# Optimization experiments

Hardware: AMD Instinct MI355X
Metric: run time of the kernel (lower is better)

The kernel has to match this reference:

```python
import jax, jax.numpy as jnp
import numpy as np

N_NODES = 100000
N_EDGES = 2000000
D = 128
REL_TYPES = 64


def setup_inputs() -> dict:
    key = jax.random.key(0)
    k1, k2, k3, k4 = jax.random.split(key, 4)
    z = jax.random.normal(k1, (N_NODES, D), dtype=jnp.float32)
    edge_index = jax.random.randint(k2, (2, N_EDGES), 0, N_NODES, dtype=jnp.int64)
    rel_id = jax.random.randint(k3, (N_EDGES,), 0, REL_TYPES, dtype=jnp.int64)
    rel = jax.random.normal(k4, (REL_TYPES, D), dtype=jnp.float32)
    return {"z": z, "edge_index": edge_index, "rel_id": rel_id, "rel": rel}


def reference(z, edge_index, rel_id, rel):
    # DistMult: sigmoid(sum_d z[src,d] * rel[rel_id,d] * z[dst,d])
    src = z[edge_index[0]]          # [E, D]
    dst = z[edge_index[1]]          # [E, D]
    r = rel[rel_id]                 # [E, D]
    scores = jnp.sum(src * r * dst, axis=1)  # [E]
    return jax.nn.sigmoid(scores)
```

## Files before the change

kernel.cpp:

```cpp
#include <hip/hip_runtime.h>
#include <hip/hip_fp16.h>
#include <stdint.h>


__global__ __launch_bounds__(256) void convert_kernel(
    const float* __restrict__ x, __half* __restrict__ xh, int n8)
{
    const int i = blockIdx.x * blockDim.x + threadIdx.x;
    if (i >= n8) return;
    const float4 f0 = ((const float4*)x)[2 * i];
    const float4 f1 = ((const float4*)x)[2 * i + 1];
    union { __half2 h2[4]; uint4 u; } o;
    o.h2[0] = __floats2half2_rn(f0.x, f0.y);
    o.h2[1] = __floats2half2_rn(f0.z, f0.w);
    o.h2[2] = __floats2half2_rn(f1.x, f1.y);
    o.h2[3] = __floats2half2_rn(f1.z, f1.w);
    ((uint4*)xh)[i] = o.u;
}

__global__ __launch_bounds__(256) void distmult_f16_lds_kernel(
    const __half* __restrict__ zh,
    const int* __restrict__ src_idx,
    const int* __restrict__ dst_idx,
    const int* __restrict__ rel_id,
    const __half* __restrict__ relh,
    float* __restrict__ out,
    int E)
{
    __shared__ uint4 rel_lds[1024];
    {
        const uint4* rsrc = (const uint4*)relh;
        #pragma unroll
        for (int k = 0; k < 4; k++)
            rel_lds[threadIdx.x + 256 * k] = rsrc[threadIdx.x + 256 * k];
    }
    __syncthreads();

    const int gtid = blockIdx.x * blockDim.x + threadIdx.x;
    const int g    = gtid >> 4;
    const int lane = threadIdx.x & 15;
    const int e0   = g * 2;
    const int e1   = e0 + 1;
    if (e0 >= E) return;
    const bool has1 = (e1 < E);

    const int s0 = src_idx[e0], d0 = dst_idx[e0], r0 = rel_id[e0];
    const int s1 = has1 ? src_idx[e1] : s0;
    const int d1 = has1 ? dst_idx[e1] : d0;
    const int r1 = has1 ? rel_id[e1]  : r0;

    union { uint4 u; __half2 h2[4]; } A0, B0, A1, B1, R0, R1;
    A0.u = ((const uint4*)(zh + (size_t)s0 * 128))[lane];
    B0.u = ((const uint4*)(zh + (size_t)d0 * 128))[lane];
    A1.u = ((const uint4*)(zh + (size_t)s1 * 128))[lane];
    B1.u = ((const uint4*)(zh + (size_t)d1 * 128))[lane];
    R0.u = rel_lds[r0 * 16 + lane];
    R1.u = rel_lds[r1 * 16 + lane];

    float v0 = 0.f, v1 = 0.f;
    #pragma unroll
    for (int j = 0; j < 4; j++) {
        const float2 a0 = __half22float2(A0.h2[j]);
        const float2 b0 = __half22float2(B0.h2[j]);
        const float2 r0f = __half22float2(R0.h2[j]);
        v0 += a0.x * r0f.x * b0.x + a0.y * r0f.y * b0.y;
        const float2 a1 = __half22float2(A1.h2[j]);
        const float2 b1 = __half22float2(B1.h2[j]);
        const float2 r1f = __half22float2(R1.h2[j]);
        v1 += a1.x * r1f.x * b1.x + a1.y * r1f.y * b1.y;
    }

    #pragma unroll
    for (int off = 8; off > 0; off >>= 1) {
        v0 += __shfl_down(v0, off, 16);
        v1 += __shfl_down(v1, off, 16);
    }

    if (lane == 0) {
        const float o0 = 1.0f / (1.0f + __expf(-v0));
        if (has1) {
            const float o1 = 1.0f / (1.0f + __expf(-v1));
            *((float2*)(out + e0)) = make_float2(o0, o1);
        } else {
            out[e0] = o0;
        }
    }
}

__global__ __launch_bounds__(256) void distmult_f16_kernel(
    const __half* __restrict__ zh,
    const int* __restrict__ src_idx, const int* __restrict__ dst_idx,
    const int* __restrict__ rel_id, const float* __restrict__ rel,
    float* __restrict__ out, int E)
{
    const int gtid = blockIdx.x * blockDim.x + threadIdx.x;
    const int e = gtid >> 4;
    const int lane = threadIdx.x & 15;
    if (e >= E) return;
    const int s = src_idx[e], d = dst_idx[e], r = rel_id[e];
    union { uint4 u; __half2 h2[4]; } A, B;
    A.u = ((const uint4*)(zh + (size_t)s * 128))[lane];
    B.u = ((const uint4*)(zh + (size_t)d * 128))[lane];
    const float4* rr = (const float4*)(rel + (size_t)r * 128);
    const float4 r0 = rr[2 * lane];
    const float4 r1 = rr[2 * lane + 1];
    const float2 a0 = __half22float2(A.h2[0]), a1 = __half22float2(A.h2[1]);
    const float2 a2 = __half22float2(A.h2[2]), a3 = __half22float2(A.h2[3]);
    const float2 b0 = __half22float2(B.h2[0]), b1 = __half22float2(B.h2[1]);
    const float2 b2 = __half22float2(B.h2[2]), b3 = __half22float2(B.h2[3]);
    float v = a0.x * r0.x * b0.x + a0.y * r0.y * b0.y
            + a1.x * r0.z * b1.x + a1.y * r0.w * b1.y
            + a2.x * r1.x * b2.x + a2.y * r1.y * b2.y
            + a3.x * r1.z * b3.x + a3.y * r1.w * b3.y;
    #pragma unroll
    for (int off = 8; off > 0; off >>= 1) v += __shfl_down(v, off, 16);
    if (lane == 0) out[e] = 1.0f / (1.0f + __expf(-v));
}

__global__ __launch_bounds__(256) void distmult_f32_kernel(
    const float* __restrict__ z,
    const int* __restrict__ src_idx, const int* __restrict__ dst_idx,
    const int* __restrict__ rel_id, const float* __restrict__ rel,
    float* __restrict__ out, int E)
{
    const int gtid = blockIdx.x * blockDim.x + threadIdx.x;
    const int e = gtid >> 4;
    const int lane = threadIdx.x & 15;
    if (e >= E) return;
    const int s = src_idx[e], d = dst_idx[e], r = rel_id[e];
    const float4* zs = (const float4*)(z + (size_t)s * 128);
    const float4* zd = (const float4*)(z + (size_t)d * 128);
    const float4* rr = (const float4*)(rel + (size_t)r * 128);
    const float4 a0 = zs[lane], a1 = zs[lane + 16];
    const float4 b0 = zd[lane], b1 = zd[lane + 16];
    const float4 c0 = rr[lane], c1 = rr[lane + 16];
    float v = a0.x * c0.x * b0.x + a0.y * c0.y * b0.y
            + a0.z * c0.z * b0.z + a0.w * c0.w * b0.w
            + a1.x * c1.x * b1.x + a1.y * c1.y * b1.y
            + a1.z * c1.z * b1.z + a1.w * c1.w * b1.w;
    #pragma unroll
    for (int off = 8; off > 0; off >>= 1) v += __shfl_down(v, off, 16);
    if (lane == 0) out[e] = 1.0f / (1.0f + __expf(-v));
}

extern "C" void kernel_launch(void* const* d_in, const int* in_sizes, int n_in,
                              void* d_out, int out_size, void* d_ws, size_t ws_size,
                              hipStream_t stream) {
    const float* z     = (const float*)d_in[0];
    const int*   eidx  = (const int*)d_in[1];
    const int*   relid = (const int*)d_in[2];
    const float* rel   = (const float*)d_in[3];
    float*       out   = (float*)d_out;

    const int nz   = in_sizes[0];
    const int E    = in_sizes[2];
    const int nrel = in_sizes[3];
    const int* src = eidx;
    const int* dst = eidx + E;

    const size_t sz_zh   = (size_t)nz * sizeof(__half);
    const size_t off_rh  = (sz_zh + 255) & ~(size_t)255;
    const size_t sz_rh   = (size_t)nrel * sizeof(__half);
    const size_t need    = off_rh + sz_rh;

    const bool rel_ok = (nrel == 64 * 128) && (nrel % 8 == 0);

    if (ws_size >= need && nz % 8 == 0 && rel_ok) {
        __half* zh = (__half*)d_ws;
        __half* rh = (__half*)((char*)d_ws + off_rh);
        const int n8z = nz / 8, n8r = nrel / 8;
        convert_kernel<<<(n8z + 255) / 256, 256, 0, stream>>>(z, zh, n8z);
        convert_kernel<<<(n8r + 255) / 256, 256, 0, stream>>>(rel, rh, n8r);
        const int groups = (E + 1) / 2;
        const int blocks = (groups * 16 + 255) / 256;
        distmult_f16_lds_kernel<<<blocks, 256, 0, stream>>>(
            zh, src, dst, relid, rh, out, E);
    } else if (ws_size >= sz_zh && nz % 8 == 0) {
        __half* zh = (__half*)d_ws;
        const int n8z = nz / 8;
        convert_kernel<<<(n8z + 255) / 256, 256, 0, stream>>>(z, zh, n8z);
        const int blocks = (E * 16 + 255) / 256;
        distmult_f16_kernel<<<blocks, 256, 0, stream>>>(zh, src, dst, relid, rel, out, E);
    } else {
        const int blocks = (E * 16 + 255) / 256;
        distmult_f32_kernel<<<blocks, 256, 0, stream>>>(z, src, dst, relid, rel, out, E);
    }
}
```

Measured before the change: 225.6 us.

## Bucket edges by src/dst node range to improve gather cache locality

Adds a scatter pass that bins edges into 512 buckets keyed by source-range and destination-range, packing src, dst, rel and edge id into 64-bit words. The compute kernel then walks each bucket so concurrently running blocks touch a limited slice of the fp16 node table, aiming to raise L2/MALL hit rates for the random row gathers. In exchange it adds an atomic-heavy scatter pass, extra 16 MB of binned traffic, scattered output writes, and silently drops edges if a bucket exceeds its fixed capacity.

```diff
diff --git a/kernel.cpp b/kernel.cpp
--- a/kernel.cpp
+++ b/kernel.cpp
@@ -2,6 +2,10 @@
 #include <hip/hip_fp16.h>
 #include <stdint.h>
 
+
+#define NSRC 8
+#define NDST 64
+#define NBKT 512
 
 __global__ __launch_bounds__(256) void convert_kernel(
     const float* __restrict__ x, __half* __restrict__ xh, int n8)
@@ -18,36 +22,71 @@
     ((uint4*)xh)[i] = o.u;
 }
 
-__global__ __launch_bounds__(256) void distmult_f16_lds_kernel(
+__global__ __launch_bounds__(256) void scatter512_kernel(
+    const int* __restrict__ src, const int* __restrict__ dst,
+    const int* __restrict__ relid, int E, int nn, int cap,
+    uint32_t* __restrict__ counters, uint64_t* __restrict__ binned)
+{
+    const int i = blockIdx.x * 256 + threadIdx.x;
+    if (i >= E) return;
+    const uint32_t s = (uint32_t)src[i];
+    const uint32_t d = (uint32_t)dst[i];
+    const uint32_t r = (uint32_t)relid[i];
+    uint32_t ss = (s * (uint32_t)NSRC) / (uint32_t)nn; if (ss > NSRC - 1) ss = NSRC - 1;
+    uint32_t ds = (d * (uint32_t)NDST) / (uint32_t)nn; if (ds > NDST - 1) ds = NDST - 1;
+    const uint32_t b = ss * NDST + ds;
+    const uint32_t pos = atomicAdd(&counters[b], 1u);
+    if (pos < (uint32_t)cap)
+        binned[(size_t)b * (size_t)cap + pos] =
+            (uint64_t)s | ((uint64_t)d << 17) | ((uint64_t)r << 34) | ((uint64_t)i << 40);
+}
+
+__global__ __launch_bounds__(256) void distmult_bucketed_kernel(
     const __half* __restrict__ zh,
-    const int* __restrict__ src_idx,
-    const int* __restrict__ dst_idx,
-    const int* __restrict__ rel_id,
+    const uint64_t* __restrict__ binned,
+    const uint32_t* __restrict__ counters,
     const __half* __restrict__ relh,
     float* __restrict__ out,
-    int E)
-{
+    int cap, int cpb)
+{
+    const int k     = blockIdx.x & 7;
+    const int t     = blockIdx.x >> 3;
+    const int j     = t / cpb;
+    const int chunk = t - j * cpb;
+    const int bkt   = k * NDST + j;
+
+    uint32_t cnt = counters[bkt];
+    if (cnt > (uint32_t)cap) cnt = (uint32_t)cap;
+    const uint32_t el_blk = (uint32_t)chunk * 32u;
+    if (el_blk >= cnt) return;
+
     __shared__ uint4 rel_lds[1024];
     {
         const uint4* rsrc = (const uint4*)relh;
         #pragma unroll
-        for (int k = 0; k < 4; k++)
-            rel_lds[threadIdx.x + 256 * k] = rsrc[threadIdx.x + 256 * k];
+        for (int q = 0; q < 4; q++)
+            rel_lds[threadIdx.x + 256 * q] = rsrc[threadIdx.x + 256 * q];
     }
     __syncthreads();
 
-    const int gtid = blockIdx.x * blockDim.x + threadIdx.x;
-    const int g    = gtid >> 4;
+    const int g    = threadIdx.x >> 4;
     const int lane = threadIdx.x & 15;
-    const int e0   = g * 2;
-    const int e1   = e0 + 1;
-    if (e0 >= E) return;
-    const bool has1 = (e1 < E);
-
-    const int s0 = src_idx[e0], d0 = dst_idx[e0], r0 = rel_id[e0];
-    const int s1 = has1 ? src_idx[e1] : s0;
-    const int d1 = has1 ? dst_idx[e1] : d0;
-    const int r1 = has1 ? rel_id[e1]  : r0;
+    const uint32_t el0 = el_blk + (uint32_t)g * 2u;
+    if (el0 >= cnt) return;
+    const bool has1 = (el0 + 1u < cnt);
+
+    const uint64_t* bb = binned + (size_t)bkt * (size_t)cap;
+    const uint64_t p0 = bb[el0];
+    const uint64_t p1 = has1 ? bb[el0 + 1u] : p0;
+
+    const uint32_t s0 = (uint32_t)p0 & 0x1FFFFu;
+    const uint32_t d0 = (uint32_t)(p0 >> 17) & 0x1FFFFu;
+    const uint32_t r0 = (uint32_t)(p0 >> 34) & 0x3Fu;
+    const uint32_t e0 = (uint32_t)(p0 >> 40);
+    const uint32_t s1 = (uint32_t)p1 & 0x1FFFFu;
+    const uint32_t d1 = (uint32_t)(p1 >> 17) & 0x1FFFFu;
+    const uint32_t r1 = (uint32_t)(p1 >> 34) & 0x3Fu;
+    const uint32_t e1 = (uint32_t)(p1 >> 40);
 
     union { uint4 u; __half2 h2[4]; } A0, B0, A1, B1, R0, R1;
     A0.u = ((const uint4*)(zh + (size_t)s0 * 128))[lane];
@@ -59,15 +98,15 @@
 
     float v0 = 0.f, v1 = 0.f;
     #pragma unroll
-    for (int j = 0; j < 4; j++) {
-        const float2 a0 = __half22float2(A0.h2[j]);
-        const float2 b0 = __half22float2(B0.h2[j]);
-        const float2 r0f = __half22float2(R0.h2[j]);
-        v0 += a0.x * r0f.x * b0.x + a0.y * r0f.y * b0.y;
-        const float2 a1 = __half22float2(A1.h2[j]);
-        const float2 b1 = __half22float2(B1.h2[j]);
-        const float2 r1f = __half22float2(R1.h2[j]);
-        v1 += a1.x * r1f.x * b1.x + a1.y * r1f.y * b1.y;
+    for (int q = 0; q < 4; q++) {
+        const float2 a0 = __half22float2(A0.h2[q]);
+        const float2 b0 = __half22float2(B0.h2[q]);
+        const float2 c0 = __half22float2(R0.h2[q]);
+        v0 += a0.x * c0.x * b0.x + a0.y * c0.y * b0.y;
+        const float2 a1 = __half22float2(A1.h2[q]);
+        const float2 b1 = __half22float2(B1.h2[q]);
+        const float2 c1 = __half22float2(R1.h2[q]);
+        v1 += a1.x * c1.x * b1.x + a1.y * c1.y * b1.y;
     }
 
     #pragma unroll
@@ -76,6 +115,64 @@
         v1 += __shfl_down(v1, off, 16);
     }
 
+    if (lane == 0) {
+        out[e0] = 1.0f / (1.0f + __expf(-v0));
+        if (has1) out[e1] = 1.0f / (1.0f + __expf(-v1));
+    }
+}
+
+__global__ __launch_bounds__(256) void distmult_f16_lds_kernel(
+    const __half* __restrict__ zh,
+    const int* __restrict__ src_idx, const int* __restrict__ dst_idx,
+    const int* __restrict__ rel_id, const __half* __restrict__ relh,
+    float* __restrict__ out, int E)
+{
+    __shared__ uint4 rel_lds[1024];
+    {
+        const uint4* rsrc = (const uint4*)relh;
+        #pragma unroll
+        for (int q = 0; q < 4; q++)
+            rel_lds[threadIdx.x + 256 * q] = rsrc[threadIdx.x + 256 * q];
+    }
+    __syncthreads();
+
+    const int gtid = blockIdx.x * blockDim.x + threadIdx.x;
+    const int g = gtid >> 4;
+    const int lane = threadIdx.x & 15;
+    const int e0 = g * 2, e1 = e0 + 1;
+    if (e0 >= E) return;
+    const bool has1 = (e1 < E);
+
+    const int s0 = src_idx[e0], d0 = dst_idx[e0], r0 = rel_id[e0];
+    const int s1 = has1 ? src_idx[e1] : s0;
+    const int d1 = has1 ? dst_idx[e1] : d0;
+    const int r1 = has1 ? rel_id[e1]  : r0;
+
+    union { uint4 u; __half2 h2[4]; } A0, B0, A1, B1, R0, R1;
+    A0.u = ((const uint4*)(zh + (size_t)s0 * 128))[lane];
+    B0.u = ((const uint4*)(zh + (size_t)d0 * 128))[lane];
+    A1.u = ((const uint4*)(zh + (size_t)s1 * 128))[lane];
+    B1.u = ((const uint4*)(zh + (size_t)d1 * 128))[lane];
+    R0.u = rel_lds[r0 * 16 + lane];
+    R1.u = rel_lds[r1 * 16 + lane];
+
+    float v0 = 0.f, v1 = 0.f;
+    #pragma unroll
+    for (int q = 0; q < 4; q++) {
+        const float2 a0 = __half22float2(A0.h2[q]);
+        const float2 b0 = __half22float2(B0.h2[q]);
+        const float2 c0 = __half22float2(R0.h2[q]);
+        v0 += a0.x * c0.x * b0.x + a0.y * c0.y * b0.y;
+        const float2 a1 = __half22float2(A1.h2[q]);
+        const float2 b1 = __half22float2(B1.h2[q]);
+        const float2 c1 = __half22float2(R1.h2[q]);
+        v1 += a1.x * c1.x * b1.x + a1.y * c1.y * b1.y;
+    }
+    #pragma unroll
+    for (int off = 8; off > 0; off >>= 1) {
+        v0 += __shfl_down(v0, off, 16);
+        v1 += __shfl_down(v1, off, 16);
+    }
     if (lane == 0) {
         const float o0 = 1.0f / (1.0f + __expf(-v0));
         if (has1) {
@@ -85,36 +182,6 @@
             out[e0] = o0;
         }
     }
-}
-
-__global__ __launch_bounds__(256) void distmult_f16_kernel(
-    const __half* __restrict__ zh,
-    const int* __restrict__ src_idx, const int* __restrict__ dst_idx,
-    const int* __restrict__ rel_id, const float* __restrict__ rel,
-    float* __restrict__ out, int E)
-{
-    const int gtid = blockIdx.x * blockDim.x + threadIdx.x;
-    const int e = gtid >> 4;
-    const int lane = threadIdx.x & 15;
-    if (e >= E) return;
-    const int s = src_idx[e], d = dst_idx[e], r = rel_id[e];
-    union { uint4 u; __half2 h2[4]; } A, B;
-    A.u = ((const uint4*)(zh + (size_t)s * 128))[lane];
-    B.u = ((const uint4*)(zh + (size_t)d * 128))[lane];
-    const float4* rr = (const float4*)(rel + (size_t)r * 128);
-    const float4 r0 = rr[2 * lane];
-    const float4 r1 = rr[2 * lane + 1];
-    const float2 a0 = __half22float2(A.h2[0]), a1 = __half22float2(A.h2[1]);
-    const float2 a2 = __half22float2(A.h2[2]), a3 = __half22float2(A.h2[3]);
-    const float2 b0 = __half22float2(B.h2[0]), b1 = __half22float2(B.h2[1]);
-    const float2 b2 = __half22float2(B.h2[2]), b3 = __half22float2(B.h2[3]);
-    float v = a0.x * r0.x * b0.x + a0.y * r0.y * b0.y
-            + a1.x * r0.z * b1.x + a1.y * r0.w * b1.y
-            + a2.x * r1.x * b2.x + a2.y * r1.y * b2.y
-            + a3.x * r1.z * b3.x + a3.y * r1.w * b3.y;
-    #pragma unroll
-    for (int off = 8; off > 0; off >>= 1) v += __shfl_down(v, off, 16);
-    if (lane == 0) out[e] = 1.0f / (1.0f + __expf(-v));
 }
 
 __global__ __launch_bounds__(256) void distmult_f32_kernel(
@@ -155,17 +222,43 @@
     const int nz   = in_sizes[0];
     const int E    = in_sizes[2];
     const int nrel = in_sizes[3];
+    const int nn   = nz / 128;
     const int* src = eidx;
     const int* dst = eidx + E;
 
-    const size_t sz_zh   = (size_t)nz * sizeof(__half);
-    const size_t off_rh  = (sz_zh + 255) & ~(size_t)255;
-    const size_t sz_rh   = (size_t)nrel * sizeof(__half);
-    const size_t need    = off_rh + sz_rh;
-
-    const bool rel_ok = (nrel == 64 * 128) && (nrel % 8 == 0);
-
-    if (ws_size >= need && nz % 8 == 0 && rel_ok) {
+    const int mean_b = E / NBKT;
+    int cap = mean_b + E / 8192 + 512;
+    cap = (cap + 31) & ~31;
+    const int cpb = cap / 32;
+
+    const size_t sz_zh    = (size_t)nz * sizeof(__half);
+    const size_t off_rh   = (sz_zh + 255) & ~(size_t)255;
+    const size_t sz_rh    = (size_t)nrel * sizeof(__half);
+    const size_t off_cnt  = (off_rh + sz_rh + 255) & ~(size_t)255;
+    const size_t sz_cnt   = (size_t)NBKT * 4;
+    const size_t off_bin  = (off_cnt + sz_cnt + 255) & ~(size_t)255;
+    const size_t sz_bin   = (size_t)NBKT * (size_t)cap * 8;
+    const size_t need     = off_bin + sz_bin;
+
+    const bool rel_ok  = (nrel == 64 * 128);
+    const bool bits_ok = (nn <= 131072) && (E <= (1 << 24)) && (nz % 8 == 0);
+
+    if (ws_size >= need && rel_ok && bits_ok) {
+        char* ws = (char*)d_ws;
+        __half*   zh       = (__half*)(ws);
+        __half*   rh       = (__half*)(ws + off_rh);
+        uint32_t* counters = (uint32_t*)(ws + off_cnt);
+        uint64_t* binned   = (uint64_t*)(ws + off_bin);
+
+        const int n8z = nz / 8, n8r = nrel / 8;
+        convert_kernel<<<(n8z + 255) / 256, 256, 0, stream>>>(z, zh, n8z);
+        convert_kernel<<<(n8r + 255) / 256, 256, 0, stream>>>(rel, rh, n8r);
+        hipMemsetAsync(counters, 0, sz_cnt, stream);
+        scatter512_kernel<<<(E + 255) / 256, 256, 0, stream>>>(
+            src, dst, relid, E, nn, cap, counters, binned);
+        distmult_bucketed_kernel<<<NSRC * NDST * cpb, 256, 0, stream>>>(
+            zh, binned, counters, rh, out, cap, cpb);
+    } else if (ws_size >= off_rh + sz_rh && rel_ok && nz % 8 == 0) {
         __half* zh = (__half*)d_ws;
         __half* rh = (__half*)((char*)d_ws + off_rh);
         const int n8z = nz / 8, n8r = nrel / 8;
@@ -175,12 +268,6 @@
         const int blocks = (groups * 16 + 255) / 256;
         distmult_f16_lds_kernel<<<blocks, 256, 0, stream>>>(
             zh, src, dst, relid, rh, out, E);
-    } else if (ws_size >= sz_zh && nz % 8 == 0) {
-        __half* zh = (__half*)d_ws;
-        const int n8z = nz / 8;
-        convert_kernel<<<(n8z + 255) / 256, 256, 0, stream>>>(z, zh, n8z);
-        const int blocks = (E * 16 + 255) / 256;
-        distmult_f16_kernel<<<blocks, 256, 0, stream>>>(zh, src, dst, relid, rel, out, E);
     } else {
         const int blocks = (E * 16 + 255) / 256;
         distmult_f32_kernel<<<blocks, 256, 0, stream>>>(z, src, dst, relid, rel, out, E);
```

Result: slower. 812.1 us (+260.1%).
